# Optimization experiments

Measured on AMD Instinct MI355X. Metric: run time of the kernel, lower is better.

## Reference

```python
import jax, jax.numpy as jnp
import numpy as np


def setup_inputs() -> dict:
    key = jax.random.key(0)
    ks = jax.random.split(key, 10)
    B, T, F, C, D, O = 4, 1000, 257, 6, 2048, 2
    # target_doas in DEGREES (module multiplies by pi/180): azi in [0,360), zenith in [0,180)
    tdoa = jax.random.uniform(ks[2], (B, T, 2), dtype=jnp.float32) * jnp.array([360.0, 180.0], jnp.float32)
    # codebook dirs in RADIANS: azi in [0,2pi), zenith in [0,pi)
    dirs = jax.random.uniform(ks[3], (D, 2), dtype=jnp.float32) * jnp.array([2.0 * np.pi, np.pi], jnp.float32)
    return {
        "X_real": jax.random.normal(ks[0], (B, T, F, C), dtype=jnp.float32),
        "X_imag": jax.random.normal(ks[1], (B, T, F, C), dtype=jnp.float32),
        "target_doas": tdoa,
        "dirs": dirs,
        "w_conj_real": jax.random.normal(ks[4], (C, F, D), dtype=jnp.float32),
        "w_conj_imag": jax.random.normal(ks[5], (C, F, D), dtype=jnp.float32),
        "w_conj_ds_real": jax.random.normal(ks[6], (C, F, D), dtype=jnp.float32),
        "w_conj_ds_imag": jax.random.normal(ks[7], (C, F, D), dtype=jnp.float32),
        "w_binaural_real": jax.random.normal(ks[8], (O, F, D), dtype=jnp.float32),
        "w_binaural_imag": jax.random.normal(ks[9], (O, F, D), dtype=jnp.float32),
    }


def _as_ri(z):
    # complex -> stacked (real, imag) float array on last axis
    return jnp.stack([jnp.real(z), jnp.imag(z)], axis=-1)


def reference(X_real, X_imag, target_doas, dirs,
              w_conj_real, w_conj_imag,
              w_conj_ds_real, w_conj_ds_imag,
              w_binaural_real, w_binaural_imag):
    # --- angular (haversine) distance to direction codebook ---
    t = (jnp.pi / 180.0) * target_doas            # [B,T,2] radians
    azi_diff = t[..., 0][:, :, None] - dirs[:, 0][None, None, :]      # [B,T,D]
    zen_diff = t[..., 1][:, :, None] - dirs[:, 1][None, None, :]      # [B,T,D]
    a = jnp.sin(zen_diff / 2) ** 2 + \
        jnp.cos(t[..., 1])[:, :, None] * jnp.cos(dirs[:, 1])[None, None, :] * jnp.sin(azi_diff / 2) ** 2
    angle_diff = 2.0 * jnp.arcsin(jnp.sqrt(jnp.clip(a, 0.0, 1.0)))
    ind = jnp.argmin(angle_diff, axis=-1)          # [B,T] nearest-codebook index

    # --- gather complex beamformer weights by index: [C,F,D] -> [B,T,F,C] ---
    def gather(w):
        return jnp.transpose(w[:, :, ind], (2, 3, 1, 0))

    X = jax.lax.complex(X_real, X_imag)                                 # [B,T,F,C]
    w_conj = jax.lax.complex(gather(w_conj_real), gather(w_conj_imag))  # [B,T,F,C]
    w_ds = jax.lax.complex(gather(w_conj_ds_real), gather(w_conj_ds_imag))
    w_bin = jax.lax.complex(gather(w_binaural_real), gather(w_binaural_imag))  # [B,T,F,O]

    ds_multichannel_out = w_ds * X                 # [B,T,F,C]
    bf_out = jnp.sum(w_conj * X, axis=-1)          # [B,T,F]
    return (_as_ri(ds_multichannel_out), _as_ri(bf_out), _as_ri(w_bin))
```

## Files before the change

### kernel.cpp

```cpp
#include <hip/hip_runtime.h>
#include <math.h>

typedef float f4v __attribute__((ext_vector_type(4)));
typedef float f2v __attribute__((ext_vector_type(2)));

constexpr int Bn = 4, Tn = 1000, Fn = 257, Cn = 6, Dn = 2048, On = 2;
constexpr int BTn = Bn * Tn;
constexpr double DEG2RAD = 0.017453292519943295;

constexpr size_t OUT0_F = (size_t)BTn * Fn * Cn * 2;
constexpr size_t OUT1_F = (size_t)BTn * Fn * 2;

constexpr int DCH = 32;
constexpr int NCH = Dn / DCH;

constexpr size_t TAB_BYTES  = (size_t)4 * Dn * sizeof(double);
constexpr size_t BTT_PAD    = 131072;
constexpr size_t IND_BYTES  = 16384;
constexpr size_t BOFF_BYTES = 4096;
constexpr size_t BENT_BYTES = 16384;
constexpr size_t WS_NEEDED  = TAB_BYTES + BTT_PAD + IND_BYTES + BOFF_BYTES + BENT_BYTES;

__global__ __launch_bounds__(256) void build_tables(const float2* __restrict__ dirs,
                                                    const float* __restrict__ tdoa,
                                                    double* __restrict__ tab,
                                                    double* __restrict__ bttab) {
    int id = blockIdx.x * 256 + threadIdx.x;
    if (id < Dn) {
        float2 dr = dirs[id];
        double d0 = (double)dr.x, d1 = (double)dr.y;
        tab[0 * Dn + id] = cos(d0);
        tab[1 * Dn + id] = sin(d0);
        tab[2 * Dn + id] = cos(d1);
        tab[3 * Dn + id] = sin(d1);
    } else if (id < Dn + BTn) {
        int bt = id - Dn;
        double t0 = DEG2RAD * (double)tdoa[bt * 2 + 0];
        double t1 = DEG2RAD * (double)tdoa[bt * 2 + 1];
        bttab[bt * 4 + 0] = cos(t0);
        bttab[bt * 4 + 1] = sin(t0);
        bttab[bt * 4 + 2] = cos(t1);
        bttab[bt * 4 + 3] = sin(t1);
    }
}

__global__ __launch_bounds__(256) void argmin_lds(const double* __restrict__ bttab,
                                                  const double* __restrict__ tab,
                                                  int* __restrict__ ind) {
    __shared__ double s_cd0[Dn];
    __shared__ double s_sd0[Dn];
    __shared__ double s_cd1[Dn];
    __shared__ double s_sd1[Dn];
    const int t = threadIdx.x;
    #pragma unroll
    for (int k = 0; k < Dn / 256; ++k) {
        int d = t + 256 * k;
        s_cd0[d] = tab[0 * Dn + d];
        s_sd0[d] = tab[1 * Dn + d];
        s_cd1[d] = tab[2 * Dn + d];
        s_sd1[d] = tab[3 * Dn + d];
    }
    __syncthreads();
    const int w = t >> 6, lane = t & 63;
    #pragma unroll
    for (int s = 0; s < 4; ++s) {
        const int bt = blockIdx.x * 16 + w * 4 + s;
        double ct0 = bttab[bt * 4 + 0], st0 = bttab[bt * 4 + 1];
        double ct1 = bttab[bt * 4 + 2], st1 = bttab[bt * 4 + 3];
        double best = 1e300;
        int bidx = 0;
        for (int i = 0; i < Dn / 256; ++i) {
            const int d0 = lane + 256 * i;
            double a[4];
            #pragma unroll
            for (int k = 0; k < 4; ++k) {
                int d = d0 + 64 * k;
                double u  = ct1 * s_cd1[d];
                double m1 = 1.0 - (u + st1 * s_sd1[d]);
                double m0 = 1.0 - (ct0 * s_cd0[d] + st0 * s_sd0[d]);
                a[k] = m1 + u * m0;
            }
            #pragma unroll
            for (int k = 0; k < 4; ++k) {
                int d = d0 + 64 * k;
                if (a[k] < best) { best = a[k]; bidx = d; }
            }
        }
        #pragma unroll
        for (int off = 32; off > 0; off >>= 1) {
            double ov = __shfl_down(best, off);
            int oi = __shfl_down(bidx, off);
            if (ov < best || (ov == best && oi < bidx)) { best = ov; bidx = oi; }
        }
        if (lane == 0) ind[bt] = bidx;
    }
}

__global__ __launch_bounds__(256) void bucket_bts(const int* __restrict__ ind,
                                                  int* __restrict__ boff,
                                                  int* __restrict__ bent) {
    __shared__ int cnts[NCH];
    __shared__ int curs[NCH];
    const int t = threadIdx.x;
    if (t < NCH) cnts[t] = 0;
    __syncthreads();
    #pragma unroll
    for (int k = 0; k < (BTn + 255) / 256; ++k) {
        int bt = k * 256 + t;
        if (bt < BTn) atomicAdd(&cnts[ind[bt] >> 5], 1);
    }
    __syncthreads();
    if (t == 0) {
        int acc = 0;
        for (int i = 0; i < NCH; ++i) { curs[i] = acc; boff[i] = acc; acc += cnts[i]; }
        boff[NCH] = acc;
    }
    __syncthreads();
    #pragma unroll
    for (int k = 0; k < (BTn + 255) / 256; ++k) {
        int bt = k * 256 + t;
        if (bt < BTn) {
            int d = ind[bt];
            int p = atomicAdd(&curs[d >> 5], 1);
            bent[p] = (bt << 5) | (d & 31);
        }
    }
}

constexpr int FCH = 8;
constexpr int RWS = FCH * Cn;

__global__ __launch_bounds__(256) void fuse_cd(
    const float* __restrict__ Xr, const float* __restrict__ Xi,
    const int* __restrict__ boff, const int* __restrict__ bent,
    const float* __restrict__ wcr, const float* __restrict__ wci,
    const float* __restrict__ wdr, const float* __restrict__ wdi,
    float* __restrict__ out0, float* __restrict__ out1) {
    __shared__ f2v tc[RWS][34];
    __shared__ f2v td[RWS][34];
    const int d0 = blockIdx.x * DCH;
    const int f0 = blockIdx.y * FCH;
    const int t = threadIdx.x;

    #pragma unroll
    for (int j = 0; j < 3; ++j) {
        int idx = j * 256 + t;
        const int pair = (idx >= 384) ? 1 : 0;
        int k = idx - pair * 384;
        int r = k >> 3, q4 = k & 7;
        int fi = r / Cn, c = r - fi * Cn;
        int f = f0 + fi;
        if (f < Fn) {
            size_t s = (size_t)(c * Fn + f) * Dn + d0 + 4 * q4;
            f4v vr = __builtin_nontemporal_load((const f4v*)((pair ? wdr : wcr) + s));
            f4v vi = __builtin_nontemporal_load((const f4v*)((pair ? wdi : wci) + s));
            f4v* trow = (f4v*)&(pair ? td : tc)[r][0];
            f4v lo = {vr[0], vi[0], vr[1], vi[1]};
            f4v hi = {vr[2], vi[2], vr[3], vi[3]};
            trow[2 * q4]     = lo;
            trow[2 * q4 + 1] = hi;
        }
    }
    const int off = boff[blockIdx.x];
    const int cnt = boff[blockIdx.x + 1] - off;
    __syncthreads();

    const int items = cnt * FCH;
    for (int base = 0; base < items; base += 256) {
        int it = base + t;
        if (it < items) {
            int m = it >> 3, fi = it & 7;
            int e = bent[off + m];
            int bt = e >> 5, dl = e & 31;
            int f = f0 + fi;
            if (f < Fn) {
                size_t xb = ((size_t)bt * Fn + f) * Cn;
                const f2v* xr2 = (const f2v*)(Xr + xb);
                const f2v* xi2 = (const f2v*)(Xi + xb);
                f2v xra = xr2[0], xrb = xr2[1], xrc = xr2[2];
                f2v xia = xi2[0], xib = xi2[1], xic = xi2[2];
                float xr[Cn] = {xra[0], xra[1], xrb[0], xrb[1], xrc[0], xrc[1]};
                float xi[Cn] = {xia[0], xia[1], xib[0], xib[1], xic[0], xic[1]};
                float o0[Cn * 2];
                float accr = 0.f, acci = 0.f;
                const int rb = fi * Cn;
                #pragma unroll
                for (int c = 0; c < Cn; ++c) {
                    f2v wcv = tc[rb + c][dl];
                    f2v wdv = td[rb + c][dl];
                    o0[2 * c]     = wdv[0] * xr[c] - wdv[1] * xi[c];
                    o0[2 * c + 1] = wdv[0] * xi[c] + wdv[1] * xr[c];
                    accr += wcv[0] * xr[c] - wcv[1] * xi[c];
                    acci += wcv[0] * xi[c] + wcv[1] * xr[c];
                }
                f4v* ob = (f4v*)(out0 + xb * 2);
                f4v p0 = {o0[0], o0[1], o0[2], o0[3]};
                f4v p1 = {o0[4], o0[5], o0[6], o0[7]};
                f4v p2 = {o0[8], o0[9], o0[10], o0[11]};
                ob[0] = p0; ob[1] = p1; ob[2] = p2;
                f2v o1 = {accr, acci};
                ((f2v*)out1)[(size_t)bt * Fn + f] = o1;
            }
        }
    }
}

constexpr int FCB = 24;
constexpr int RWB = FCB * On;

__global__ __launch_bounds__(256) void fuse_b(
    const int* __restrict__ boff, const int* __restrict__ bent,
    const float* __restrict__ wbr, const float* __restrict__ wbi,
    float* __restrict__ out2) {
    __shared__ f2v tb[RWB][34];
    const int d0 = blockIdx.x * DCH;
    const int f0 = blockIdx.y * FCB;
    const int t = threadIdx.x;

    #pragma unroll
    for (int j = 0; j < 2; ++j) {
        int idx = j * 256 + t;
        if (idx < RWB * 8) {
            int r = idx >> 3, q4 = idx & 7;
            int fi = r >> 1, o = r & 1;
            int f = f0 + fi;
            if (f < Fn) {
                size_t s = (size_t)(o * Fn + f) * Dn + d0 + 4 * q4;
                f4v vr = __builtin_nontemporal_load((const f4v*)(wbr + s));
                f4v vi = __builtin_nontemporal_load((const f4v*)(wbi + s));
                f4v* trow = (f4v*)&tb[r][0];
                f4v lo = {vr[0], vi[0], vr[1], vi[1]};
                f4v hi = {vr[2], vi[2], vr[3], vi[3]};
                trow[2 * q4]     = lo;
                trow[2 * q4 + 1] = hi;
            }
        }
    }
    const int off = boff[blockIdx.x];
    const int cnt = boff[blockIdx.x + 1] - off;
    __syncthreads();

    const int items = cnt * FCB;
    for (int base = 0; base < items; base += 256) {
        int it = base + t;
        if (it < items) {
            int m = it / FCB, fi = it - m * FCB;
            int e = bent[off + m];
            int bt = e >> 5, dl = e & 31;
            int f = f0 + fi;
            if (f < Fn) {
                f2v a = tb[fi * 2][dl];
                f2v b = tb[fi * 2 + 1][dl];
                f4v o2 = {a[0], a[1], b[0], b[1]};
                ((f4v*)out2)[(size_t)bt * Fn + f] = o2;
            }
        }
    }
}

__global__ __launch_bounds__(256) void main_direct(
    const float* __restrict__ Xr, const float* __restrict__ Xi,
    const float* __restrict__ tdoa, const float2* __restrict__ dirs,
    const float* __restrict__ wcr, const float* __restrict__ wci,
    const float* __restrict__ wdr, const float* __restrict__ wdi,
    const float* __restrict__ wbr, const float* __restrict__ wbi,
    float2* __restrict__ out0, float2* __restrict__ out1, float2* __restrict__ out2) {
    const int bt = blockIdx.x;
    const int tid = threadIdx.x;
    __shared__ double sv[256];
    __shared__ int si[256];

    double t0 = DEG2RAD * (double)tdoa[bt * 2 + 0];
    double t1 = DEG2RAD * (double)tdoa[bt * 2 + 1];
    double ct1 = cos(t1);
    double best = 1e300;
    int bidx = 0;
    for (int d = tid; d < Dn; d += 256) {
        float2 dr = dirs[d];
        double s1 = sin(0.5 * (t1 - (double)dr.y));
        double s2 = sin(0.5 * (t0 - (double)dr.x));
        double a = s1 * s1 + ct1 * cos((double)dr.y) * (s2 * s2);
        if (a < best) { best = a; bidx = d; }
    }
    sv[tid] = best; si[tid] = bidx;
    __syncthreads();
    for (int s = 128; s > 0; s >>= 1) {
        if (tid < s) {
            double v = sv[tid + s]; int j = si[tid + s];
            if (v < sv[tid] || (v == sv[tid] && j < si[tid])) { sv[tid] = v; si[tid] = j; }
        }
        __syncthreads();
    }
    const int dsel = si[0];
    const size_t base = (size_t)bt * Fn * Cn;

    for (int f = tid; f < Fn; f += 256) {
        const int fc = f * Cn;
        float accr = 0.f, acci = 0.f;
        #pragma unroll
        for (int c = 0; c < Cn; ++c) {
            float xr = Xr[base + fc + c], xi = Xi[base + fc + c];
            size_t wo = (size_t)(c * Fn + f) * Dn + dsel;
            float a_ = wdr[wo], b_ = wdi[wo];
            out0[base + fc + c] = make_float2(a_ * xr - b_ * xi, a_ * xi + b_ * xr);
            float p = wcr[wo], q = wci[wo];
            accr += p * xr - q * xi;
            acci += p * xi + q * xr;
        }
        out1[(size_t)bt * Fn + f] = make_float2(accr, acci);
        #pragma unroll
        for (int o = 0; o < On; ++o) {
            size_t wo = (size_t)(o * Fn + f) * Dn + dsel;
            out2[((size_t)bt * Fn + f) * On + o] = make_float2(wbr[wo], wbi[wo]);
        }
    }
}

extern "C" void kernel_launch(void* const* d_in, const int* in_sizes, int n_in,
                              void* d_out, int out_size, void* d_ws, size_t ws_size,
                              hipStream_t stream) {
    const float* Xr   = (const float*)d_in[0];
    const float* Xi   = (const float*)d_in[1];
    const float* tdoa = (const float*)d_in[2];
    const float2* dirs = (const float2*)d_in[3];
    const float* wcr = (const float*)d_in[4];
    const float* wci = (const float*)d_in[5];
    const float* wdr = (const float*)d_in[6];
    const float* wdi = (const float*)d_in[7];
    const float* wbr = (const float*)d_in[8];
    const float* wbi = (const float*)d_in[9];

    float* out = (float*)d_out;

    if (ws_size >= WS_NEEDED) {
        char* ws = (char*)d_ws;
        double* tab   = (double*)ws;
        double* bttab = (double*)(ws + TAB_BYTES);
        int* ind  = (int*)(ws + TAB_BYTES + BTT_PAD);
        int* boff = (int*)(ws + TAB_BYTES + BTT_PAD + IND_BYTES);
        int* bent = (int*)(ws + TAB_BYTES + BTT_PAD + IND_BYTES + BOFF_BYTES);

        build_tables<<<(Dn + BTn + 255) / 256, 256, 0, stream>>>(dirs, tdoa, tab, bttab);
        argmin_lds<<<BTn / 16, 256, 0, stream>>>(bttab, tab, ind);
        bucket_bts<<<1, 256, 0, stream>>>(ind, boff, bent);
        dim3 gcd(NCH, (Fn + FCH - 1) / FCH);
        fuse_cd<<<gcd, 256, 0, stream>>>(Xr, Xi, boff, bent, wcr, wci, wdr, wdi,
                                         out, out + OUT0_F);
        dim3 gb(NCH, (Fn + FCB - 1) / FCB);
        fuse_b<<<gb, 256, 0, stream>>>(boff, bent, wbr, wbi, out + OUT0_F + OUT1_F);
    } else {
        main_direct<<<BTn, 256, 0, stream>>>(Xr, Xi, tdoa, dirs,
                                             wcr, wci, wdr, wdi, wbr, wbi,
                                             (float2*)out,
                                             (float2*)(out + OUT0_F),
                                             (float2*)(out + OUT0_F + OUT1_F));
    }
}
```

Baseline: 69.67 us.

## Merge fuse_cd and fuse_b into one launch and prefetch X loads ahead

Combines the two gather kernels into a single grid whose y-dimension picks either the beamformer/delay-sum path or the binaural path, which removes one kernel launch and its tail. In the main path, the first X loads are issued before the weight-tile staging, and the next iteration's X loads are software-pipelined so their latency overlaps with the current compute. It also drops the nontemporal hints on weight loads. The cost is more register pressure and a larger shared allocation for the binaural blocks.

```diff
diff --git a/kernel.cpp b/kernel.cpp
--- a/kernel.cpp
+++ b/kernel.cpp
@@ -13,6 +13,12 @@
 
 constexpr int DCH = 32;
 constexpr int NCH = Dn / DCH;
+constexpr int FCH = 8;
+constexpr int RWS = FCH * Cn;
+constexpr int FCB = 24;
+constexpr int RWB = FCB * On;
+constexpr int YCD = (Fn + FCH - 1) / FCH;
+constexpr int YB  = (Fn + FCB - 1) / FCB;
 
 constexpr size_t TAB_BYTES  = (size_t)4 * Dn * sizeof(double);
 constexpr size_t BTT_PAD    = 131072;
@@ -127,132 +133,143 @@
     }
 }
 
-constexpr int FCH = 8;
-constexpr int RWS = FCH * Cn;
-
-__global__ __launch_bounds__(256) void fuse_cd(
+__global__ __launch_bounds__(256) void fuse_all(
     const float* __restrict__ Xr, const float* __restrict__ Xi,
     const int* __restrict__ boff, const int* __restrict__ bent,
     const float* __restrict__ wcr, const float* __restrict__ wci,
     const float* __restrict__ wdr, const float* __restrict__ wdi,
-    float* __restrict__ out0, float* __restrict__ out1) {
-    __shared__ f2v tc[RWS][34];
-    __shared__ f2v td[RWS][34];
-    const int d0 = blockIdx.x * DCH;
-    const int f0 = blockIdx.y * FCH;
+    const float* __restrict__ wbr, const float* __restrict__ wbi,
+    float* __restrict__ out0, float* __restrict__ out1, float* __restrict__ out2) {
+    __shared__ __align__(16) char smem[2 * RWS * 34 * sizeof(f2v)];
+    const int bx = blockIdx.x;
+    const int d0 = bx * DCH;
     const int t = threadIdx.x;
-
-    #pragma unroll
-    for (int j = 0; j < 3; ++j) {
-        int idx = j * 256 + t;
-        const int pair = (idx >= 384) ? 1 : 0;
-        int k = idx - pair * 384;
-        int r = k >> 3, q4 = k & 7;
-        int fi = r / Cn, c = r - fi * Cn;
-        int f = f0 + fi;
-        if (f < Fn) {
-            size_t s = (size_t)(c * Fn + f) * Dn + d0 + 4 * q4;
-            f4v vr = __builtin_nontemporal_load((const f4v*)((pair ? wdr : wcr) + s));
-            f4v vi = __builtin_nontemporal_load((const f4v*)((pair ? wdi : wci) + s));
-            f4v* trow = (f4v*)&(pair ? td : tc)[r][0];
-            f4v lo = {vr[0], vi[0], vr[1], vi[1]};
-            f4v hi = {vr[2], vi[2], vr[3], vi[3]};
-            trow[2 * q4]     = lo;
-            trow[2 * q4 + 1] = hi;
-        }
-    }
-    const int off = boff[blockIdx.x];
-    const int cnt = boff[blockIdx.x + 1] - off;
-    __syncthreads();
-
-    const int items = cnt * FCH;
-    for (int base = 0; base < items; base += 256) {
-        int it = base + t;
-        if (it < items) {
-            int m = it >> 3, fi = it & 7;
-            int e = bent[off + m];
-            int bt = e >> 5, dl = e & 31;
+    const int off = boff[bx];
+    const int cnt = boff[bx + 1] - off;
+
+    if (blockIdx.y < YCD) {
+        f2v (*tc)[34] = (f2v(*)[34])smem;
+        f2v (*td)[34] = (f2v(*)[34])(smem + sizeof(f2v) * RWS * 34);
+        const int f0 = blockIdx.y * FCH;
+        const int items = cnt * FCH;
+
+        bool vA = false; int btA = 0, fA = 0, dlA = 0, rbA = 0;
+        f2v xrA0 = {0,0}, xrA1 = {0,0}, xrA2 = {0,0};
+        f2v xiA0 = {0,0}, xiA1 = {0,0}, xiA2 = {0,0};
+        if (t < items) {
+            int e = bent[off + (t >> 3)];
+            int fi = t & 7, f = f0 + fi;
+            if (f < Fn) {
+                vA = true; btA = e >> 5; fA = f; dlA = e & 31; rbA = fi * Cn;
+                size_t xb = ((size_t)btA * Fn + f) * Cn;
+                const f2v* xr2 = (const f2v*)(Xr + xb);
+                const f2v* xi2 = (const f2v*)(Xi + xb);
+                xrA0 = xr2[0]; xrA1 = xr2[1]; xrA2 = xr2[2];
+                xiA0 = xi2[0]; xiA1 = xi2[1]; xiA2 = xi2[2];
+            }
+        }
+        #pragma unroll
+        for (int j = 0; j < 3; ++j) {
+            int idx = j * 256 + t;
+            const int pair = (idx >= 384) ? 1 : 0;
+            int k = idx - pair * 384;
+            int r = k >> 3, q4 = k & 7;
+            int fi = r / Cn, c = r - fi * Cn;
             int f = f0 + fi;
             if (f < Fn) {
-                size_t xb = ((size_t)bt * Fn + f) * Cn;
-                const f2v* xr2 = (const f2v*)(Xr + xb);
-                const f2v* xi2 = (const f2v*)(Xi + xb);
-                f2v xra = xr2[0], xrb = xr2[1], xrc = xr2[2];
-                f2v xia = xi2[0], xib = xi2[1], xic = xi2[2];
-                float xr[Cn] = {xra[0], xra[1], xrb[0], xrb[1], xrc[0], xrc[1]};
-                float xi[Cn] = {xia[0], xia[1], xib[0], xib[1], xic[0], xic[1]};
+                size_t s = (size_t)(c * Fn + f) * Dn + d0 + 4 * q4;
+                f4v vr = *(const f4v*)((pair ? wdr : wcr) + s);
+                f4v vi = *(const f4v*)((pair ? wdi : wci) + s);
+                f4v* trow = (f4v*)&(pair ? td : tc)[r][0];
+                f4v lo = {vr[0], vi[0], vr[1], vi[1]};
+                f4v hi = {vr[2], vi[2], vr[3], vi[3]};
+                trow[2 * q4]     = lo;
+                trow[2 * q4 + 1] = hi;
+            }
+        }
+        __syncthreads();
+
+        for (int base = 0; base < items; base += 256) {
+            bool vB = false; int btB = 0, fB = 0, dlB = 0, rbB = 0;
+            f2v xrB0 = {0,0}, xrB1 = {0,0}, xrB2 = {0,0};
+            f2v xiB0 = {0,0}, xiB1 = {0,0}, xiB2 = {0,0};
+            int itn = base + 256 + t;
+            if (itn < items) {
+                int e = bent[off + (itn >> 3)];
+                int fi = itn & 7, f = f0 + fi;
+                if (f < Fn) {
+                    vB = true; btB = e >> 5; fB = f; dlB = e & 31; rbB = fi * Cn;
+                    size_t xb = ((size_t)btB * Fn + f) * Cn;
+                    const f2v* xr2 = (const f2v*)(Xr + xb);
+                    const f2v* xi2 = (const f2v*)(Xi + xb);
+                    xrB0 = xr2[0]; xrB1 = xr2[1]; xrB2 = xr2[2];
+                    xiB0 = xi2[0]; xiB1 = xi2[1]; xiB2 = xi2[2];
+                }
+            }
+            if (vA) {
+                float xr[Cn] = {xrA0[0], xrA0[1], xrA1[0], xrA1[1], xrA2[0], xrA2[1]};
+                float xi[Cn] = {xiA0[0], xiA0[1], xiA1[0], xiA1[1], xiA2[0], xiA2[1]};
                 float o0[Cn * 2];
                 float accr = 0.f, acci = 0.f;
-                const int rb = fi * Cn;
                 #pragma unroll
                 for (int c = 0; c < Cn; ++c) {
-                    f2v wcv = tc[rb + c][dl];
-                    f2v wdv = td[rb + c][dl];
+                    f2v wcv = tc[rbA + c][dlA];
+                    f2v wdv = td[rbA + c][dlA];
                     o0[2 * c]     = wdv[0] * xr[c] - wdv[1] * xi[c];
                     o0[2 * c + 1] = wdv[0] * xi[c] + wdv[1] * xr[c];
                     accr += wcv[0] * xr[c] - wcv[1] * xi[c];
                     acci += wcv[0] * xi[c] + wcv[1] * xr[c];
                 }
+                size_t xb = ((size_t)btA * Fn + fA) * Cn;
                 f4v* ob = (f4v*)(out0 + xb * 2);
                 f4v p0 = {o0[0], o0[1], o0[2], o0[3]};
                 f4v p1 = {o0[4], o0[5], o0[6], o0[7]};
                 f4v p2 = {o0[8], o0[9], o0[10], o0[11]};
                 ob[0] = p0; ob[1] = p1; ob[2] = p2;
                 f2v o1 = {accr, acci};
-                ((f2v*)out1)[(size_t)bt * Fn + f] = o1;
-            }
-        }
-    }
-}
-
-constexpr int FCB = 24;
-constexpr int RWB = FCB * On;
-
-__global__ __launch_bounds__(256) void fuse_b(
-    const int* __restrict__ boff, const int* __restrict__ bent,
-    const float* __restrict__ wbr, const float* __restrict__ wbi,
-    float* __restrict__ out2) {
-    __shared__ f2v tb[RWB][34];
-    const int d0 = blockIdx.x * DCH;
-    const int f0 = blockIdx.y * FCB;
-    const int t = threadIdx.x;
-
-    #pragma unroll
-    for (int j = 0; j < 2; ++j) {
-        int idx = j * 256 + t;
-        if (idx < RWB * 8) {
-            int r = idx >> 3, q4 = idx & 7;
-            int fi = r >> 1, o = r & 1;
-            int f = f0 + fi;
-            if (f < Fn) {
-                size_t s = (size_t)(o * Fn + f) * Dn + d0 + 4 * q4;
-                f4v vr = __builtin_nontemporal_load((const f4v*)(wbr + s));
-                f4v vi = __builtin_nontemporal_load((const f4v*)(wbi + s));
-                f4v* trow = (f4v*)&tb[r][0];
-                f4v lo = {vr[0], vi[0], vr[1], vi[1]};
-                f4v hi = {vr[2], vi[2], vr[3], vi[3]};
-                trow[2 * q4]     = lo;
-                trow[2 * q4 + 1] = hi;
-            }
-        }
-    }
-    const int off = boff[blockIdx.x];
-    const int cnt = boff[blockIdx.x + 1] - off;
-    __syncthreads();
-
-    const int items = cnt * FCB;
-    for (int base = 0; base < items; base += 256) {
-        int it = base + t;
-        if (it < items) {
-            int m = it / FCB, fi = it - m * FCB;
-            int e = bent[off + m];
-            int bt = e >> 5, dl = e & 31;
-            int f = f0 + fi;
-            if (f < Fn) {
-                f2v a = tb[fi * 2][dl];
-                f2v b = tb[fi * 2 + 1][dl];
-                f4v o2 = {a[0], a[1], b[0], b[1]};
-                ((f4v*)out2)[(size_t)bt * Fn + f] = o2;
+                ((f2v*)out1)[(size_t)btA * Fn + fA] = o1;
+            }
+            vA = vB; btA = btB; fA = fB; dlA = dlB; rbA = rbB;
+            xrA0 = xrB0; xrA1 = xrB1; xrA2 = xrB2;
+            xiA0 = xiB0; xiA1 = xiB1; xiA2 = xiB2;
+        }
+    } else {
+        f2v (*tb)[34] = (f2v(*)[34])smem;
+        const int f0 = (blockIdx.y - YCD) * FCB;
+        #pragma unroll
+        for (int j = 0; j < 2; ++j) {
+            int idx = j * 256 + t;
+            if (idx < RWB * 8) {
+                int r = idx >> 3, q4 = idx & 7;
+                int fi = r >> 1, o = r & 1;
+                int f = f0 + fi;
+                if (f < Fn) {
+                    size_t s = (size_t)(o * Fn + f) * Dn + d0 + 4 * q4;
+                    f4v vr = *(const f4v*)(wbr + s);
+                    f4v vi = *(const f4v*)(wbi + s);
+                    f4v* trow = (f4v*)&tb[r][0];
+                    f4v lo = {vr[0], vi[0], vr[1], vi[1]};
+                    f4v hi = {vr[2], vi[2], vr[3], vi[3]};
+                    trow[2 * q4]     = lo;
+                    trow[2 * q4 + 1] = hi;
+                }
+            }
+        }
+        __syncthreads();
+        const int items = cnt * FCB;
+        for (int base = 0; base < items; base += 256) {
+            int it = base + t;
+            if (it < items) {
+                int m = it / FCB, fi = it - m * FCB;
+                int e = bent[off + m];
+                int bt = e >> 5, dl = e & 31;
+                int f = f0 + fi;
+                if (f < Fn) {
+                    f2v a = tb[fi * 2][dl];
+                    f2v b = tb[fi * 2 + 1][dl];
+                    f4v o2 = {a[0], a[1], b[0], b[1]};
+                    ((f4v*)out2)[(size_t)bt * Fn + f] = o2;
+                }
             }
         }
     }
@@ -343,11 +360,10 @@
         build_tables<<<(Dn + BTn + 255) / 256, 256, 0, stream>>>(dirs, tdoa, tab, bttab);
         argmin_lds<<<BTn / 16, 256, 0, stream>>>(bttab, tab, ind);
         bucket_bts<<<1, 256, 0, stream>>>(ind, boff, bent);
-        dim3 gcd(NCH, (Fn + FCH - 1) / FCH);
-        fuse_cd<<<gcd, 256, 0, stream>>>(Xr, Xi, boff, bent, wcr, wci, wdr, wdi,
-                                         out, out + OUT0_F);
-        dim3 gb(NCH, (Fn + FCB - 1) / FCB);
-        fuse_b<<<gb, 256, 0, stream>>>(boff, bent, wbr, wbi, out + OUT0_F + OUT1_F);
+        dim3 g(NCH, YCD + YB);
+        fuse_all<<<g, 256, 0, stream>>>(Xr, Xi, boff, bent,
+                                        wcr, wci, wdr, wdi, wbr, wbi,
+                                        out, out + OUT0_F, out + OUT0_F + OUT1_F);
     } else {
         main_direct<<<BTn, 256, 0, stream>>>(Xr, Xi, tdoa, dirs,
                                              wcr, wci, wdr, wdi, wbr, wbi,
```

Result: faster. 60.97 us (-12.5%).
